# Kernel optimization log

Measured on AMD Instinct MI355X. Metric: run time of the kernel, lower is better.

Reference implementation:

```python
import jax, jax.numpy as jnp
import numpy as np

SL, BS, OUT_SL = 64, 64, 48
NH, EME, EMD = 256, 512, 768   # em_sz_dec == 3*NH required by copy-score reshape/bmm
VE, VD = 32000, 32000
NL = 2


def setup_inputs() -> dict:
    key = jax.random.key(0)
    ks = iter(jax.random.split(key, 32))
    def W(*s, sc=0.05):
        return jax.random.normal(next(ks), s, jnp.float32) * sc
    inp = jax.random.randint(next(ks), (SL, BS), 0, VE)
    y = jax.random.randint(next(ks), (SL, BS), 0, VD)
    return dict(
        inp=inp, y=y,
        emb_enc=W(VE, EME, sc=0.1),
        enc_Wih=W(NL, 2, 3 * NH, EME), enc_Whh=W(NL, 2, 3 * NH, NH),
        enc_bih=W(NL, 2, 3 * NH), enc_bhh=W(NL, 2, 3 * NH),
        out_enc_W=W(EMD, 2 * NH),
        emb_dec=W(VD, EMD, sc=0.1),
        dec_Wih=W(NL, 3 * EMD, EMD), dec_Whh=W(NL, 3 * EMD, EMD),
        dec_bih=W(NL, 3 * EMD), dec_bhh=W(NL, 3 * EMD),
        out_b=W(VD),
        W1=W(2 * NH, EMD), l2_W=W(EMD, EMD), l2_b=W(EMD),
        l3_W=W(EMD, EMD + 2 * NH), l3_b=W(EMD),
        Vp=W(EMD),
    )


def _gru_cell(x, h, Wih, Whh, bih, bhh):
    # torch nn.GRU cell equations
    gi = x @ Wih.T + bih
    gh = h @ Whh.T + bhh
    ir, iz, inn = jnp.split(gi, 3, axis=-1)
    hr, hz, hn = jnp.split(gh, 3, axis=-1)
    r = jax.nn.sigmoid(ir + hr)
    z = jax.nn.sigmoid(iz + hz)
    n = jnp.tanh(inn + r * hn)
    return (1.0 - z) * n + z * h


def _gru_layer(xs, h0, Wih, Whh, bih, bhh, reverse=False):
    def step(h, x):
        h2 = _gru_cell(x, h, Wih, Whh, bih, bhh)
        return h2, h2
    hT, ys = jax.lax.scan(step, h0, xs, reverse=reverse)
    return ys, hT


def reference(inp, y, emb_enc, enc_Wih, enc_Whh, enc_bih, enc_bhh, out_enc_W,
              emb_dec, dec_Wih, dec_Whh, dec_bih, dec_bhh, out_b,
              W1, l2_W, l2_b, l3_W, l3_b, Vp):
    sl, bs = inp.shape
    # ---- encoder: 2-layer bidirectional GRU ----
    x = emb_enc[inp]                                   # (sl, bs, EME)
    h_fin = []
    for l in range(NL):
        yf, hf = _gru_layer(x, jnp.zeros((bs, NH), x.dtype),
                            enc_Wih[l, 0], enc_Whh[l, 0], enc_bih[l, 0], enc_bhh[l, 0])
        yb, hb = _gru_layer(x, jnp.zeros((bs, NH), x.dtype),
                            enc_Wih[l, 1], enc_Whh[l, 1], enc_bih[l, 1], enc_bhh[l, 1],
                            reverse=True)
        x = jnp.concatenate([yf, yb], -1)              # (sl, bs, 2*NH)
        h_fin.append(jnp.concatenate([hf, hb], -1))    # (bs, 2*NH)
    enc_out = x
    # h.view(2,2,bs,-1).permute(0,2,1,3).view(2,bs,-1) == per-layer [fwd,bwd] concat
    h = jnp.stack(h_fin) @ out_enc_W.T                 # (2, bs, EMD)

    w1e = enc_out @ W1                                 # (sl, bs, EMD)
    sc_base = jnp.tanh(enc_out @ out_enc_W.T).transpose(1, 0, 2)  # (bs, sl, EMD)
    yT = y.T                                           # (bs, sl) copy indices
    Vsz = emb_dec.shape[0]
    row = jnp.arange(bs)[:, None]
    # dec_inp: step 0 uses zeros token, then teacher-forced y[i-1]
    dec_inputs = jnp.concatenate([jnp.zeros((1, bs), y.dtype), y[:OUT_SL - 1]], 0)

    def step(h, dec_t):
        # Bahdanau attention
        w2h = h[-1] @ l2_W.T + l2_b                    # (bs, EMD)
        u = jnp.tanh(w1e + w2h[None])                  # (sl, bs, EMD)
        a = jax.nn.softmax(u @ Vp, axis=0)             # (sl, bs)
        Xa = jnp.einsum('sb,sbe->be', a, enc_out)      # (bs, 2*NH)
        e = emb_dec[dec_t]                             # (bs, EMD)
        wgt = jnp.concatenate([e, Xa], -1) @ l3_W.T + l3_b
        # 2-layer decoder GRU, single step
        h0n = _gru_cell(wgt, h[0], dec_Wih[0], dec_Whh[0], dec_bih[0], dec_bhh[0])
        h1n = _gru_cell(h0n, h[1], dec_Wih[1], dec_Whh[1], dec_bih[1], dec_bhh[1])
        hn = jnp.stack([h0n, h1n])
        dec_out = h1n                                  # (bs, EMD)
        outp = dec_out @ emb_dec.T + out_b             # generate scores (bs, VD), tied weights
        score_c = jnp.tanh(jnp.einsum('bse,be->bs', sc_base, dec_out))  # copy scores (bs, sl)
        probs = jax.nn.softmax(jnp.concatenate([outp, score_c], 1), axis=1)  # (bs, VD+sl)
        prob_g = probs[:, :Vsz]
        prob_c = probs[:, Vsz:]
        # scatter-add copy probs onto the token ids of y (the copy mechanism)
        out1 = jnp.zeros_like(probs).at[row, yT].add(prob_c)
        out1 = out1.at[:, :Vsz].add(prob_g)
        return hn, out1

    _, res = jax.lax.scan(step, h, dec_inputs)         # (OUT_SL, bs, VD+sl)
    return res
```

## Files before the change

kernel.cpp:

```cpp
#include <hip/hip_runtime.h>

#define SLEN 64
#define BSZ  64
#define TSL  48
#define VDIM 32000
#define NCOL 32064

typedef __attribute__((ext_vector_type(8))) _Float16 f16x8;
typedef __attribute__((ext_vector_type(4))) _Float16 f16x4;
typedef __attribute__((ext_vector_type(4))) float f32x4;

__device__ __forceinline__ float fsig(float x){
    return 1.0f/(1.0f + __expf(-x));
}
__device__ __forceinline__ float ftanh(float x){
    float e = __expf(2.0f*x);
    return 1.0f - 2.0f/(e + 1.0f);
}
__device__ __forceinline__ unsigned short f2h(float x){
    union { _Float16 f; unsigned short u; } c; c.f = (_Float16)x; return c.u;
}
__device__ __forceinline__ float h2f(unsigned short u){
    union { _Float16 f; unsigned short u; } c; c.u = u; return (float)c.f;
}
// ... 226 lines not shown
    for (int g = 0; g < 3; ++g) acc[g] = (f32x4){0.f,0.f,0.f,0.f};

    const float* Ar = A + (size_t)arow*K + kof;
    const int brow_n = colg16 + (ln & 15);
    const int Khalf = K >> 1;
    const int kbeg = kh * Khalf;

    #pragma unroll 2
    for (int k0 = kbeg; k0 < kbeg + Khalf; k0 += 32) {
        float4 a0 = *reinterpret_cast<const float4*>(Ar + k0);
        float4 a1 = *reinterpret_cast<const float4*>(Ar + k0 + 4);
        f16x8 ah, al;
        {
            float av0=a0.x, av1=a0.y, av2=a0.z, av3=a0.w;
            float av4=a1.x, av5=a1.y, av6=a1.z, av7=a1.w;
            _Float16 hh;
            hh=(_Float16)av0; ah[0]=hh; al[0]=(_Float16)(av0-(float)hh);
            hh=(_Float16)av1; ah[1]=hh; al[1]=(_Float16)(av1-(float)hh);
            hh=(_Float16)av2; ah[2]=hh; al[2]=(_Float16)(av2-(float)hh);
            hh=(_Float16)av3; ah[3]=hh; al[3]=(_Float16)(av3-(float)hh);
            hh=(_Float16)av4; ah[4]=hh; al[4]=(_Float16)(av4-(float)hh);
            hh=(_Float16)av5; ah[5]=hh; al[5]=(_Float16)(av5-(float)hh);
            hh=(_Float16)av6; ah[6]=hh; al[6]=(_Float16)(av6-(float)hh);
            hh=(_Float16)av7; ah[7]=hh; al[7]=(_Float16)(av7-(float)hh);
        }
        #pragma unroll
        for (int g = 0; g < 3; ++g) {
            const size_t boff = (size_t)(g*768 + brow_n)*K + k0 + kof;
            f16x8 bh = *reinterpret_cast<const f16x8*>(&BH[boff]);
            acc[g] = __builtin_amdgcn_mfma_f32_16x16x32_f16(ah, bh, acc[g], 0,0,0);
            acc[g] = __builtin_amdgcn_mfma_f32_16x16x32_f16(al, bh, acc[g], 0,0,0);
            if (has_lo) {
                f16x8 bl = *reinterpret_cast<const f16x8*>(&BL[boff]);
                acc[g] = __builtin_amdgcn_mfma_f32_16x16x32_f16(ah, bl, acc[g], 0,0,0);
            }
        }
    }

    __shared__ float red[4][64][12];
    if (kh == 1) {
        #pragma unroll
        for (int g = 0; g < 3; ++g)
            #pragma unroll
            for (int j = 0; j < 4; ++j) red[rw][ln][g*4 + j] = acc[g][j];
    }
    __syncthreads();
    if (kh == 1) return;
    #pragma unroll
    for (int g = 0; g < 3; ++g)
        #pragma unroll
        for (int j = 0; j < 4; ++j) acc[g][j] += red[rw][ln][g*4 + j];

    const int colg = colg16 + (ln & 15);
    const int rb   = rw*16 + (ln >> 4)*4;
    if (gate) {
        const float br = bias[colg], bz = bias[768+colg], bn = bias[1536+colg];
        #pragma unroll
        for (int jj = 0; jj < 4; ++jj) {
            const int row = rb + jj;
            float er = 0.f, ez = 0.f, en = 0.f;
            if (E) {
                er = h2f(E[(size_t)row*2304 + colg]);
                ez = h2f(E[(size_t)row*2304 + 768 + colg]);
                en = h2f(E[(size_t)row*2304 + 1536 + colg]);
            }
            float ghr = gh[(size_t)row*2304 + colg];
            float ghz = gh[(size_t)row*2304 + 768 + colg];
            float ghn = gh[(size_t)row*2304 + 1536 + colg];
            float h   = hold[(size_t)row*768 + colg];
            outp[(size_t)row*768 + colg] =
                gru_fuse(acc[0][jj]+br+er, acc[1][jj]+bz+ez, acc[2][jj]+bn+en, ghr, ghz, ghn, h);
        }
    } else {
        #pragma unroll
        for (int g = 0; g < 3; ++g) {
            const float bz = bias[g*768 + colg];
            #pragma unroll
            for (int jj = 0; jj < 4; ++jj)
                outp[(size_t)(rb+jj)*2304 + g*768 + colg] = acc[g][jj] + bz;
        }
    }
}

__global__ __launch_bounds__(512) void vocab4_k(
    const float* __restrict__ A,
    const unsigned short* __restrict__ B0, const float* __restrict__ bias0,
    unsigned short* __restrict__ scr16, float* __restrict__ psum,
    const unsigned short* __restrict__ B1, const float* __restrict__ bias1, float* __restrict__ C1,
    const unsigned short* __restrict__ B2, const float* __restrict__ bias2, float* __restrict__ C2,
    const unsigned short* __restrict__ scb16, float* __restrict__ cpt)
{
    const int z = blockIdx.z;
    const int t = threadIdx.x, w = t >> 6, ln = t & 63;

    if (z == 3) {
        const int b = blockIdx.x;
        if (b >= 64) return;
        __shared__ float hsh[768];
        for (int i = t; i < 768; i += 512) hsh[i] = A[(size_t)b*768 + i];
        __syncthreads();
        for (int ss = 0; ss < 8; ++ss) {
            const int s = w*8 + ss;
            const unsigned short* sp = scb16 + (size_t)(b*64 + s)*768;
            float acc = 0.f;
            #pragma unroll
            for (int q = 0; q < 6; ++q) {
                int e = ln*2 + q*128;
                unsigned u = *reinterpret_cast<const unsigned*>(&sp[e]);
                acc += h2f((unsigned short)(u & 0xffff))*hsh[e]
                     + h2f((unsigned short)(u >> 16))*hsh[e+1];
            }
            for (int off = 32; off; off >>= 1) acc += __shfl_down(acc, off);
            if (ln == 0) cpt[b*64 + s] = ftanh(acc);
        }
        return;
    }

    const unsigned short* Bh; const float* bias; int N, ldc;
    if (z == 0)      { Bh=B0; bias=bias0; N=VDIM; ldc=VDIM; }
    else if (z == 1) { Bh=B1; bias=bias1; N=768;  ldc=768; }
    else             { Bh=B2; bias=bias2; N=2304; ldc=2304; }
    const int n0 = blockIdx.x * 128;
    if (n0 >= N) return;

    __shared__ __align__(16) unsigned short As[2][64][72];
    __shared__ __align__(16) unsigned short Bs[128][72];
    __shared__ float rs[4][64];

    const int cw = w & 3;
    const int mh = w >> 2;

    f32x4 acc[2][2];
    #pragma unroll
    for (int i = 0; i < 2; ++i)
        #pragma unroll
        for (int j = 0; j < 2; ++j) acc[i][j] = (f32x4){0.f,0.f,0.f,0.f};

    for (int k0 = 0; k0 < 768; k0 += 64) {
        __syncthreads();
        #pragma unroll
        for (int it = 0; it < 2; ++it) {
            int idx = t + it*512;
            int r = idx >> 4, c4 = (idx & 15) * 4;
            float4 v = *reinterpret_cast<const float4*>(A + (size_t)r*768 + k0 + c4);
            ushort4 h, l; float rm;
            h.x = f2h_hi(v.x, rm); l.x = f2h(rm);
            h.y = f2h_hi(v.y, rm); l.y = f2h(rm);
            h.z = f2h_hi(v.z, rm); l.z = f2h(rm);
            h.w = f2h_hi(v.w, rm); l.w = f2h(rm);
            *reinterpret_cast<ushort4*>(&As[0][r][c4]) = h;
            *reinterpret_cast<ushort4*>(&As[1][r][c4]) = l;
        }
        #pragma unroll
        for (int it = 0; it < 2; ++it) {
            int idx = t + it*512;
            int r = idx >> 3, c8 = (idx & 7) * 8;
            *reinterpret_cast<uint4*>(&Bs[r][c8]) =
                *reinterpret_cast<const uint4*>(&Bh[(size_t)(n0+r)*768 + k0 + c8]);
        }
        __syncthreads();
        #pragma unroll
        for (int ks = 0; ks < 2; ++ks) {
            const int ko = ks*32 + (ln >> 4)*8;
            f16x8 ah[2], al[2], bh[2];
            #pragma unroll
            for (int m = 0; m < 2; ++m) {
                ah[m] = *reinterpret_cast<const f16x8*>(&As[0][mh*32 + m*16 + (ln&15)][ko]);
                al[m] = *reinterpret_cast<const f16x8*>(&As[1][mh*32 + m*16 + (ln&15)][ko]);
            }
            #pragma unroll
            for (int n = 0; n < 2; ++n)
                bh[n] = *reinterpret_cast<const f16x8*>(&Bs[cw*32 + n*16 + (ln&15)][ko]);
            #pragma unroll
            for (int m = 0; m < 2; ++m)
                #pragma unroll
                for (int n = 0; n < 2; ++n) {
                    acc[m][n] = __builtin_amdgcn_mfma_f32_16x16x32_f16(ah[m], bh[n], acc[m][n], 0,0,0);
                    acc[m][n] = __builtin_amdgcn_mfma_f32_16x16x32_f16(al[m], bh[n], acc[m][n], 0,0,0);
                }
        }
    }

    if (z == 0) {
        __syncthreads();
        unsigned short (*Cs)[128] = reinterpret_cast<unsigned short(*)[128]>(&As[0][0][0]);
        float sums[2][4];
        #pragma unroll
        for (int m = 0; m < 2; ++m)
            #pragma unroll
            for (int j = 0; j < 4; ++j) sums[m][j] = 0.f;
        #pragma unroll
        for (int m = 0; m < 2; ++m) {
            #pragma unroll
            for (int n = 0; n < 2; ++n) {
                const int cl = cw*32 + n*16 + (ln & 15);
                const float bz = bias[n0 + cl];
                #pragma unroll
                for (int j = 0; j < 4; ++j) {
                    const int row = mh*32 + m*16 + (ln >> 4)*4 + j;
                    float e = __expf(acc[m][n][j] + bz);
                    Cs[row][cl] = f2h(e);
                    sums[m][j] += e;
                }
            }
        }
        #pragma unroll
        for (int m = 0; m < 2; ++m)
            #pragma unroll
            for (int j = 0; j < 4; ++j) {
                float v = sums[m][j];
                v += __shfl_xor(v, 1); v += __shfl_xor(v, 2);
                v += __shfl_xor(v, 4); v += __shfl_xor(v, 8);
                if ((ln & 15) == 0)
                    rs[cw][mh*32 + m*16 + (ln >> 4)*4 + j] = v;
            }
        __syncthreads();
        #pragma unroll
        for (int it = 0; it < 2; ++it) {
            int jj = t + it*512;
            int row = jj >> 4, c8 = (jj & 15) * 8;
            *reinterpret_cast<uint4*>(&scr16[(size_t)row*VDIM + n0 + c8]) =
                *reinterpret_cast<const uint4*>(&Cs[row][c8]);
        }
        if (t < 64)
            atomicAdd(&psum[t*8 + (blockIdx.x & 7)], rs[0][t]+rs[1][t]+rs[2][t]+rs[3][t]);
    } else {
        float* C = (z == 1) ? C1 : C2;
        #pragma unroll
        for (int m = 0; m < 2; ++m) {
            #pragma unroll
            for (int n = 0; n < 2; ++n) {
                const int col = n0 + cw*32 + n*16 + (ln & 15);
                const float bz = bias[col];
                #pragma unroll
                for (int j = 0; j < 4; ++j) {
                    const int row = mh*32 + m*16 + (ln >> 4)*4 + j;
                    C[(size_t)row*ldc + col] = acc[m][n][j] + bz;
                }
            }
        }
    }
}

__global__ __launch_bounds__(512) void attsm_k(
    const unsigned short* __restrict__ w1e16, const float* __restrict__ w2h,
    const float* __restrict__ Vp, const unsigned short* __restrict__ enc16,
    const int* __restrict__ y,
    int step, int do_att, int do_sm,
    float* __restrict__ wgt_in,
    const unsigned short* __restrict__ scr16, const float* __restrict__ cpt,
    const float* __restrict__ psum, float* __restrict__ outprev)
{
    const int b = blockIdx.x, t = threadIdx.x;
    const int w = t >> 6, ln = t & 63;
    if (blockIdx.y == 0) {
        if (!do_att) return;
        __shared__ float w2s[768];
        __shared__ float vps[768];
        __shared__ float aa[64];
        for (int i = t; i < 768; i += 512) { w2s[i] = w2h[(size_t)b*768 + i]; vps[i] = Vp[i]; }
        __syncthreads();
        for (int ss = 0; ss < 8; ++ss) {
            const int s = w*8 + ss;
            const unsigned short* wrow = w1e16 + (size_t)(b*64 + s)*768;
            float acc = 0.f;
            #pragma unroll
            for (int q = 0; q < 6; ++q) {
                int e = ln*2 + q*128;
                unsigned u = *reinterpret_cast<const unsigned*>(&wrow[e]);
                acc += ftanh(h2f((unsigned short)(u & 0xffff)) + w2s[e])*vps[e]
                     + ftanh(h2f((unsigned short)(u >> 16))   + w2s[e+1])*vps[e+1];
            }
            for (int off = 32; off; off >>= 1) acc += __shfl_down(acc, off);
            if (ln == 0) aa[s] = acc;
        }
        __syncthreads();
        if (t < 64) {
            float v = aa[t];
            float m = v;
            for (int off = 32; off; off >>= 1) m = fmaxf(m, __shfl_xor(m, off));
            float e = __expf(v - m);
            float ssum = e;
            for (int off = 32; off; off >>= 1) ssum += __shfl_xor(ssum, off);
            aa[t] = e / ssum;
        }
        __syncthreads();
        {
            float a0 = 0.f;
            const unsigned short* ebase = enc16 + (size_t)(b*64)*512 + t;
            #pragma unroll 8
            for (int s = 0; s < 64; ++s)
                a0 += aa[s] * h2f(ebase[(size_t)s*512]);
            wgt_in[(size_t)b*512 + t] = a0;
        }
    } else {
        if (!do_sm) return;
        __shared__ float cps[64];
        __shared__ float invS;
        if (t < 64) cps[t] = __expf(cpt[b*64 + t]);
        __syncthreads();
        if (t < 64) {
            float v = cps[t];
            for (int off = 32; off; off >>= 1) v += __shfl_xor(v, off);
            if (t == 0) {
                float tot = v;
                #pragma unroll
                for (int k = 0; k < 8; ++k) tot += psum[b*8 + k];
                invS = 1.0f / tot;
            }
        }
        __syncthreads();
        const float inv = invS;
        const unsigned short* srow = scr16 + (size_t)b*VDIM;
        float* orow = outprev + (size_t)b*NCOL;
        for (int i = t*8; i < VDIM; i += 4096) {
            uint4 u = *reinterpret_cast<const uint4*>(&srow[i]);
            float4 o0, o1;
            o0.x = h2f((unsigned short)(u.x & 0xffff))*inv; o0.y = h2f((unsigned short)(u.x >> 16))*inv;
            o0.z = h2f((unsigned short)(u.y & 0xffff))*inv; o0.w = h2f((unsigned short)(u.y >> 16))*inv;
            o1.x = h2f((unsigned short)(u.z & 0xffff))*inv; o1.y = h2f((unsigned short)(u.z >> 16))*inv;
            o1.z = h2f((unsigned short)(u.w & 0xffff))*inv; o1.w = h2f((unsigned short)(u.w >> 16))*inv;
            *reinterpret_cast<float4*>(&orow[i])     = o0;
            *reinterpret_cast<float4*>(&orow[i + 4]) = o1;
        }
        if (t >= 448) orow[VDIM + (t - 448)] = 0.0f;
        __syncthreads();
        if (t < 64) atomicAdd(&orow[y[t*64 + b]], cps[t] * inv);
    }
}

__global__ __launch_bounds__(256) void convhl_k(
    const float* __restrict__ W, unsigned short* __restrict__ hi,
    unsigned short* __restrict__ lo, int n4)
{
    int i = blockIdx.x*256 + threadIdx.x;
    if (i >= n4) return;
    float4 v = reinterpret_cast<const float4*>(W)[i];
    ushort4 h, l; float r;
    h.x = f2h_hi(v.x, r); l.x = f2h(r);
    h.y = f2h_hi(v.y, r); l.y = f2h(r);
    h.z = f2h_hi(v.z, r); l.z = f2h(r);
    h.w = f2h_hi(v.w, r); l.w = f2h(r);
    reinterpret_cast<ushort4*>(hi)[i] = h;
    reinterpret_cast<ushort4*>(lo)[i] = l;
}
__global__ __launch_bounds__(256) void conv16_k(
    const float* __restrict__ W, unsigned short* __restrict__ hi, int n4)
{
    int i = blockIdx.x*256 + threadIdx.x;
    if (i >= n4) return;
    float4 v = reinterpret_cast<const float4*>(W)[i];
    ushort4 h;
    h.x = f2h(v.x); h.y = f2h(v.y); h.z = f2h(v.z); h.w = f2h(v.w);
    reinterpret_cast<ushort4*>(hi)[i] = h;
}
__global__ __launch_bounds__(256) void convw03_k(
    const float* __restrict__ W03f, unsigned short* __restrict__ We,
    unsigned short* __restrict__ Wx)
{
    int i = blockIdx.x*256 + threadIdx.x;
    if (i >= 2304*320) return;
    int r = i / 320, c4 = (i - r*320) * 4;
    float4 v = *reinterpret_cast<const float4*>(W03f + (size_t)r*1280 + c4);
    ushort4 h;
    h.x = f2h(v.x); h.y = f2h(v.y); h.z = f2h(v.z); h.w = f2h(v.w);
    if (c4 < 768)
        *reinterpret_cast<ushort4*>(&We[(size_t)r*768 + c4]) = h;
    else
        *reinterpret_cast<ushort4*>(&Wx[(size_t)r*512 + (c4 - 768)]) = h;
}
__global__ __launch_bounds__(256) void embrows_k(
    const int* __restrict__ y, const float* __restrict__ emb_dec,
    float* __restrict__ Ag)
{
    int i = blockIdx.x*256 + threadIdx.x;
    if (i >= 3072*192) return;
    int row = i / 192, c4 = (i - row*192) * 4;
    int tok = (row < 64) ? 0 : y[row - 64];
    *reinterpret_cast<float4*>(Ag + (size_t)row*768 + c4) =
        *reinterpret_cast<const float4*>(emb_dec + (size_t)tok*768 + c4);
}
__global__ __launch_bounds__(256) void transpose2_k(
    const float* __restrict__ S, float* __restrict__ D, int R, int C)
{
    int i = blockIdx.x*256 + threadIdx.x;
    if (i >= R*C) return;
    int r = i / C, c = i - r*C;
    D[(size_t)c*R + r] = S[i];
}
__global__ __launch_bounds__(256) void b03_k(
    const float* __restrict__ Wih0, const float* __restrict__ bih0,
    const float* __restrict__ l3b, float* __restrict__ b03)
{
    int j = blockIdx.x*256 + threadIdx.x;
    if (j >= 2304) return;
    const float* wr = Wih0 + (size_t)j*768;
    float s = 0.f;
    #pragma unroll 4
    for (int m = 0; m < 768; m += 4) {
        float4 w = *reinterpret_cast<const float4*>(wr + m);
        float4 b = *reinterpret_cast<const float4*>(l3b + m);
        s += w.x*b.x + w.y*b.y + w.z*b.z + w.w*b.w;
    }
    b03[j] = bih0[j] + s;
}

__global__ __launch_bounds__(256) void embed_k(const int* inp, const float* emb, float* x)
{
    int i = blockIdx.x*256 + threadIdx.x;
    if (i >= 4096*128) return;
// ... 247 lines not shown
        const int s = wv*16 + ss;
        const float* sp = scb + (size_t)(b*64 + s)*768;
        float acc = 0.f;
        #pragma unroll
        for (int q = 0; q < 12; ++q) { int e = ln + q*64; acc += sp[e]*hsh[e]; }
        for (int off = 32; off; off >>= 1) acc += __shfl_down(acc, off);
        if (ln == 0) cps[s] = ftanh(acc);
    }
    __syncthreads();

    const float* row = scratch + (size_t)b*VDIM;
    float m = -1e30f;
    for (int i = t; i < VDIM; i += 256) m = fmaxf(m, row[i]);
    for (int off = 32; off; off >>= 1) m = fmaxf(m, __shfl_xor(m, off));
    if (ln == 0) red[wv] = m;
    __syncthreads();
    const float bm = fmaxf(fmaxf(red[0], red[1]), fmaxf(red[2], red[3]));
    __syncthreads();

    float s = 0.f;
    for (int i = t; i < VDIM; i += 256) s += __expf(row[i] - bm);
    if (t < 64) s += __expf(cps[t] - bm);
    for (int off = 32; off; off >>= 1) s += __shfl_xor(s, off);
    if (ln == 0) red[wv] = s;
    __syncthreads();
    const float inv = 1.0f / (red[0] + red[1] + red[2] + red[3]);

    float* orow = out + (size_t)b*NCOL;
    for (int i = t; i < VDIM; i += 256) orow[i] = __expf(row[i] - bm) * inv;
    if (t >= 192) orow[VDIM + (t - 192)] = 0.0f;
    __syncthreads();
    if (t < 64) atomicAdd(&orow[y[t*64 + b]], __expf(cps[t] - bm) * inv);
}

extern "C" void kernel_launch(void* const* d_in, const int* in_sizes, int n_in,
                              void* d_out, int out_size, void* d_ws, size_t ws_size,
                              hipStream_t stream)
{
    (void)in_sizes; (void)n_in; (void)out_size;
    const int*   inp       = (const int*)  d_in[0];
    const int*   y         = (const int*)  d_in[1];
    const float* emb_enc   = (const float*)d_in[2];
    const float* enc_Wih   = (const float*)d_in[3];
    const float* enc_Whh   = (const float*)d_in[4];
    const float* enc_bih   = (const float*)d_in[5];
    const float* enc_bhh   = (const float*)d_in[6];
    const float* out_enc_W = (const float*)d_in[7];
    const float* emb_dec   = (const float*)d_in[8];
    const float* dec_Wih   = (const float*)d_in[9];
    const float* dec_Whh   = (const float*)d_in[10];
    const float* dec_bih   = (const float*)d_in[11];
    const float* dec_bhh   = (const float*)d_in[12];
    const float* out_b     = (const float*)d_in[13];
    const float* W1        = (const float*)d_in[14];
    const float* l2_W      = (const float*)d_in[15];
    const float* l2_b      = (const float*)d_in[16];
    const float* l3_W      = (const float*)d_in[17];
    const float* l3_b      = (const float*)d_in[18];
    const float* Vp        = (const float*)d_in[19];
    float* out = (float*)d_out;
    float* ws  = (float*)d_ws;

    size_t off = 0;
    auto alloc = [&](size_t n) { float* p = ws + off; off += (n + 63) & ~(size_t)63; return p; };
    float* x0     = alloc(4096*512);
    float* x1     = alloc(4096*512);
    float* x2     = alloc(4096*512);
    float* giF    = alloc(4096*768);
    float* giB    = alloc(4096*768);
    float* w1e    = alloc(4096*768);
    float* scb    = alloc(4096*768);
    float* W1T    = alloc(768*512);
    float* hfin   = alloc(128*512);
    float* hdecA  = alloc(128*768);
    float* hdecB  = alloc(128*768);
    float* w2h    = alloc(64*768);
    float* wgt_in = alloc(64*1280);
    float* wgt    = alloc(64*768);
    float* gh0buf = alloc(64*2304);
    float* gh1buf = alloc(64*2304);
    float* gi0f   = alloc(64*2304);
    float* gi1f   = alloc(64*2304);
    float* b03    = alloc(2304);
    float* psum   = alloc(512);
    float* cpt    = alloc(64*64);
    float* scratch= alloc(64*VDIM);
    auto ualloc = [&](size_t nush) { return (unsigned short*)alloc((nush + 1) / 2); };
    unsigned short* encWhhH = ualloc(2*2*768*256);
    unsigned short* encWhhP = ualloc(2*3*32*256*8);
    unsigned short* embH    = ualloc((size_t)VDIM*768);
    unsigned short* encWihH = ualloc(2*2*768*512);
    unsigned short* encWihL = ualloc(2*2*768*512);
    unsigned short* W1TH    = ualloc(768*512);
    unsigned short* W1TL    = ualloc(768*512);
    unsigned short* oeH     = ualloc(768*512);
    unsigned short* oeL     = ualloc(768*512);
    unsigned short* l2H     = ualloc(768*768);
    unsigned short* l3TH    = ualloc(1280*768);
    unsigned short* l3TL    = ualloc(1280*768);
    unsigned short* dWihH   = ualloc((size_t)2*2304*768);
    unsigned short* dWhhH   = ualloc((size_t)2*2304*768);
    unsigned short* W03eH   = ualloc((size_t)2304*768);
    unsigned short* W03xH   = ualloc((size_t)2304*512);
    unsigned short* Egi16   = ualloc((size_t)3072*2304);
    const bool use_mfma = ws_size >= off * sizeof(float);

    const size_t L1W = (size_t)2304*768;
    float* l3T  = scratch;
    float* W03f = x0;
    float* Ag   = x0;
    unsigned short* scr16 = (unsigned short*)scratch;
    unsigned short* w1e16 = (unsigned short*)giF;
    unsigned short* enc16 = (unsigned short*)(giF + 1600*1024);
    unsigned short* scb16 = (unsigned short*)giB;

    embed_k<<<2048, 256, 0, stream>>>(inp, emb_enc, x0);
    transpose2_k<<<(512*768 + 255)/256, 256, 0, stream>>>(W1, W1T, 512, 768);
    conv16_k<<<768, 256, 0, stream>>>(enc_Whh, encWhhH, 2*2*768*256/4);

    if (use_mfma) {
        packwhh_k<<<192, 256, 0, stream>>>(enc_Whh, encWhhP);
        convhl_k<<<1536, 256, 0, stream>>>(enc_Wih, encWihH, encWihL, 2*2*768*512/4);
        convhl_k<<<384, 256, 0, stream>>>(W1T, W1TH, W1TL, 768*512/4);
        convhl_k<<<384, 256, 0, stream>>>(out_enc_W, oeH, oeL, 768*512/4);
        conv16_k<<<576, 256, 0, stream>>>(l2_W, l2H, 768*768/4);
        conv16_k<<<3456, 256, 0, stream>>>(dec_Wih, dWihH, (int)(L1W*2/4));
        conv16_k<<<3456, 256, 0, stream>>>(dec_Whh, dWhhH, (int)(L1W*2/4));
        conv16_k<<<24000, 256, 0, stream>>>(emb_dec, embH, (int)((size_t)VDIM*768/4));
        transpose2_k<<<(768*1280 + 255)/256, 256, 0, stream>>>(l3_W, l3T, 768, 1280);
        convhl_k<<<960, 256, 0, stream>>>(l3T, l3TH, l3TL, 1280*768/4);
        b03_k<<<9, 256, 0, stream>>>(dec_Wih, dec_bih, l3_b, b03);

        for (int l = 0; l < 2; ++l) {
            const float* xin  = l ? x1 : x0;
            float*       xout = l ? x2 : x1;
            const size_t wo = (size_t)l*2*768*512;
            mfma_gemm<<<dim3(6, 64, 2), 256, 0, stream>>>(
                xin, encWihH + wo,           encWihL + wo,           enc_bih + l*2*768,       giF, 768, 768, 0,
                xin, encWihH + wo + 768*512, encWihL + wo + 768*512, enc_bih + l*2*768 + 768, giB, 768, 768, 0,
                512, 0);
            enc_cp_k<<<dim3(64, 2), 256, 0, stream>>>(
                giF, giB, encWhhP, enc_bhh + (size_t)l*2*768,
                xout, hfin + (size_t)l*64*512, l);
            if (l == 0)
                packwhh_k<<<192, 256, 0, stream>>>(enc_Whh + (size_t)2*768*256, encWhhP);
        }

        mfma_gemm<<<dim3(10, 36, 1), 256, 0, stream>>>(
            dec_Wih, l3TH, l3TL, nullptr, W03f, 1280, 1280, 0,
            nullptr, nullptr, nullptr, nullptr, nullptr, 0, 0, 0,
            768, 0);
        convw03_k<<<(2304*320 + 255)/256, 256, 0, stream>>>(W03f, W03eH, W03xH);

        embrows_k<<<(3072*192 + 255)/256, 256, 0, stream>>>(y, emb_dec, Ag);
        mfma_gemm<<<dim3(18, 48, 1), 256, 0, stream>>>(
            Ag, W03eH, nullptr, nullptr, (float*)Egi16, 2304, 2304, 0,
            nullptr, nullptr, nullptr, nullptr, nullptr, 0, 0, 0,
            768, 1);

        mfma_gemm<<<dim3(6, 2, 1), 256, 0, stream>>>(
            hfin, oeH, oeL, nullptr, hdecA, 768, 768, 0,
            nullptr, nullptr, nullptr, nullptr, nullptr, 0, 0, 0,
            512, 0);

        mfma_gemm<<<dim3(6, 64, 2), 256, 0, stream>>>(
            x2, W1TH, W1TL, nullptr, w1e, 768, 768, 0,
            x2, oeH,  oeL,  nullptr, scb, 768, 768, 1,
            512, 0);

        conv16_k<<<3072, 256, 0, stream>>>(w1e, w1e16, 4096*768/4);
        conv16_k<<<3072, 256, 0, stream>>>(scb, scb16, 4096*768/4);
        conv16_k<<<2048, 256, 0, stream>>>(x2, enc16, 4096*512/4);

        mfma_gemm<<<dim3(6, 1, 1), 256, 0, stream>>>(
            hdecA + 64*768, l2H, nullptr, l2_b, w2h, 768, 768, 0,
            nullptr, nullptr, nullptr, nullptr, nullptr, 0, 0, 0,
            768, 0);
        gru_mfma_k<<<dim3(48, 1, 2), 512, 0, stream>>>(
            hdecA,          dWhhH,       nullptr, dec_bhh,        nullptr, nullptr, gh0buf, 0, 768, nullptr,
            hdecA + 64*768, dWhhH + L1W, nullptr, dec_bhh + 2304, nullptr, nullptr, gh1buf, 0, 768, nullptr,
            nullptr);

        for (int st = 0; st < TSL; ++st) {
            float* h0c = (st & 1) ? hdecB : hdecA;
            float* h0n = (st & 1) ? hdecA : hdecB;
            float* h1c = h0c + 64*768;
            float* h1n = h0n + 64*768;
            float* oprev = out + (size_t)(st > 0 ? st - 1 : 0)*BSZ*NCOL;

            attsm_k<<<dim3(64, 2), 512, 0, stream>>>(
                w1e16, w2h, Vp, enc16, y, st, 1, (st > 0) ? 1 : 0,
                wgt_in, scr16, cpt, psum, oprev);

            gru_mfma_k<<<dim3(48, 1, 1), 512, 0, stream>>>(
                wgt_in, W03xH, nullptr, b03, gh0buf, h0c, h0n, 1, 512, Egi16 + (size_t)st*64*2304,
                wgt_in, W03xH, nullptr, b03, gh0buf, h0c, h0n, 1, 512, Egi16 + (size_t)st*64*2304,
                psum);

            gru_mfma_k<<<dim3(48, 1, 2), 512, 0, stream>>>(
                h0n, dWihH + L1W, nullptr, dec_bih + 2304, gh1buf, h1c, h1n, 1, 768, nullptr,
                h0n, dWhhH,       nullptr, dec_bhh,        nullptr, nullptr, gh0buf, 0, 768, nullptr,
                nullptr);

            vocab4_k<<<dim3(250, 1, 4), 512, 0, stream>>>(
                h1n,
                embH, out_b, scr16, psum,
                l2H, l2_b, w2h,
                dWhhH + L1W, dec_bhh + 2304, gh1buf,
                scb16, cpt);
        }
        attsm_k<<<dim3(64, 2), 512, 0, stream>>>(
            w1e16, w2h, Vp, enc16, y, TSL, 0, 1,
            wgt_in, scr16, cpt, psum, out + (size_t)(TSL-1)*BSZ*NCOL);
    } else {
        for (int l = 0; l < 2; ++l) {
            const float* xin  = l ? x1 : x0;
            float*       xout = l ? x2 : x1;
            const float* Wih = enc_Wih + (size_t)l*2*768*512;
            const float* bih = enc_bih + (size_t)l*2*768;
            gemm64<<<dim3(12, 64, 2), 256, 0, stream>>>(
                xin, Wih,           bih,       giF, 0,
                xin, Wih + 768*512, bih + 768, giB, 0,
                4096, 768, 512, 768);
            enc_layer4_k<<<dim3(16, 2), 256, 0, stream>>>(
                giF, giB, encWhhH + (size_t)l*2*768*256, enc_bhh + (size_t)l*2*768,
                xout, hfin + (size_t)l*64*512, l);
        }
        gemm64<<<dim3(12, 2, 1), 256, 0, stream>>>(
            hfin, out_enc_W, nullptr, hdecA, 0,
            hfin, out_enc_W, nullptr, hdecA, 0,
            128, 768, 512, 768);
        gemm64<<<dim3(12, 64, 2), 256, 0, stream>>>(
            x2, W1T,       nullptr, w1e, 0,
            x2, out_enc_W, nullptr, scb, 1,
            4096, 768, 512, 768);
        gemm_skinny<<<dim3(12, 4, 1), 256, 0, stream>>>(
            hdecA + 64*768, l2_W, l2_b, w2h,
            hdecA + 64*768, l2_W, l2_b, w2h,
            768, 768, 768);

        for (int st = 0; st < TSL; ++st) {
            float* h0c = (st & 1) ? hdecB : hdecA;
            float* h0n = (st & 1) ? hdecA : hdecB;
            float* h1c = h0c + 64*768;
            float* h1n = h0n + 64*768;
            float* orow = out + (size_t)st*BSZ*NCOL;

            att_fused_k<<<64, 256, 0, stream>>>(w1e, w2h, Vp, x2, emb_dec, y, st, wgt_in);
            gemm_skinny<<<dim3(12, 4, 1), 256, 0, stream>>>(
                wgt_in, l3_W, l3_b, wgt,
                wgt_in, l3_W, l3_b, wgt,
                768, 1280, 768);
            gemm_skinny<<<dim3(36, 4, 2), 256, 0, stream>>>(
                wgt, dec_Wih, dec_bih, gi0f,
                h0c, dec_Whh, dec_bhh, gh0buf,
                2304, 768, 2304);
            gru_gate_k<<<192, 256, 0, stream>>>(gi0f, gh0buf, h0c, h0n);
            gemm_skinny<<<dim3(36, 4, 2), 256, 0, stream>>>(
                h0n, dec_Wih + L1W, dec_bih + 2304, gi1f,
                h1c, dec_Whh + L1W, dec_bhh + 2304, gh1buf,
                2304, 768, 2304);
            gru_gate_k<<<192, 256, 0, stream>>>(gi1f, gh1buf, h1c, h1n);
            gemm_skinny<<<dim3(12, 4, 1), 256, 0, stream>>>(
                h1n, l2_W, l2_b, w2h,
                h1n, l2_W, l2_b, w2h,
                768, 768, 768);
            gemm64<<<dim3(500, 1, 1), 256, 0, stream>>>(
                h1n, emb_dec, out_b, scratch, 0,
                h1n, emb_dec, out_b, scratch, 0,
                64, VDIM, 768, VDIM);
            smax2_k<<<64, 256, 0, stream>>>(scratch, scb, h1n, y, orow);
        }
    }
}
```

Before: 5.063 ms.

## Software-pipeline vocab GEMM one step behind and fuse it with attention

Moves the large vocab-projection GEMM out of the per-step tail kernel and into a merged kernel that runs next step's attention and the previous step's softmax normalisation/scatter in the same launch. The vocab GEMM for step st-1 now overlaps with attention for step st, and normalisation lags two steps, so scratch, psum and copy-score buffers are double-buffered. The aim is to shorten the serial critical path of the decoder loop by letting the independent vocab work fill the GPU during the small latency-bound attention and GRU kernels. It costs a second 64x32000 fp16 scratch buffer and two extra drain launches after the loop.

```diff
diff --git a/kernel.cpp b/kernel.cpp
--- a/kernel.cpp
+++ b/kernel.cpp
@@ -332,20 +332,217 @@
     }
 }
 
-__global__ __launch_bounds__(512) void vocab4_k(
+__global__ __launch_bounds__(512) void mega_k(
+    const float* __restrict__ hv, const unsigned short* __restrict__ embH,
+    const float* __restrict__ out_b,
+    unsigned short* __restrict__ scrW, float* __restrict__ psumW,
+    const unsigned short* __restrict__ w1e16, const float* __restrict__ w2h,
+    const float* __restrict__ Vp, const unsigned short* __restrict__ enc16,
+    float* __restrict__ wgt_in,
+    const unsigned short* __restrict__ scrR, const float* __restrict__ cptR,
+    const float* __restrict__ psumR,
+    const int* __restrict__ y, float* __restrict__ outprev,
+    int do_vocab, int do_att, int do_sm)
+{
+    __shared__ __align__(16) unsigned short As[2][64][72];
+    __shared__ __align__(16) unsigned short Bs[128][72];
+    __shared__ float rs[4][64];
+    const int bid = blockIdx.x;
+    const int t = threadIdx.x, w = t >> 6, ln = t & 63;
+
+    if (bid < 250) {
+        if (!do_vocab) return;
+        const int n0 = bid * 128;
+        const int cw = w & 3, mh = w >> 2;
+
+        f32x4 acc[2][2];
+        #pragma unroll
+        for (int i = 0; i < 2; ++i)
+            #pragma unroll
+            for (int j = 0; j < 2; ++j) acc[i][j] = (f32x4){0.f,0.f,0.f,0.f};
+
+        for (int k0 = 0; k0 < 768; k0 += 64) {
+            __syncthreads();
+            #pragma unroll
+            for (int it = 0; it < 2; ++it) {
+                int idx = t + it*512;
+                int r = idx >> 4, c4 = (idx & 15) * 4;
+                float4 v = *reinterpret_cast<const float4*>(hv + (size_t)r*768 + k0 + c4);
+                ushort4 h, l; float rm;
+                h.x = f2h_hi(v.x, rm); l.x = f2h(rm);
+                h.y = f2h_hi(v.y, rm); l.y = f2h(rm);
+                h.z = f2h_hi(v.z, rm); l.z = f2h(rm);
+                h.w = f2h_hi(v.w, rm); l.w = f2h(rm);
+                *reinterpret_cast<ushort4*>(&As[0][r][c4]) = h;
+                *reinterpret_cast<ushort4*>(&As[1][r][c4]) = l;
+            }
+            #pragma unroll
+            for (int it = 0; it < 2; ++it) {
+                int idx = t + it*512;
+                int r = idx >> 3, c8 = (idx & 7) * 8;
+                *reinterpret_cast<uint4*>(&Bs[r][c8]) =
+                    *reinterpret_cast<const uint4*>(&embH[(size_t)(n0+r)*768 + k0 + c8]);
+            }
+            __syncthreads();
+            #pragma unroll
+            for (int ks = 0; ks < 2; ++ks) {
+                const int ko = ks*32 + (ln >> 4)*8;
+                f16x8 ah[2], al[2], bh[2];
+                #pragma unroll
+                for (int m = 0; m < 2; ++m) {
+                    ah[m] = *reinterpret_cast<const f16x8*>(&As[0][mh*32 + m*16 + (ln&15)][ko]);
+                    al[m] = *reinterpret_cast<const f16x8*>(&As[1][mh*32 + m*16 + (ln&15)][ko]);
+                }
+                #pragma unroll
+                for (int n = 0; n < 2; ++n)
+                    bh[n] = *reinterpret_cast<const f16x8*>(&Bs[cw*32 + n*16 + (ln&15)][ko]);
+                #pragma unroll
+                for (int m = 0; m < 2; ++m)
+                    #pragma unroll
+                    for (int n = 0; n < 2; ++n) {
+                        acc[m][n] = __builtin_amdgcn_mfma_f32_16x16x32_f16(ah[m], bh[n], acc[m][n], 0,0,0);
+                        acc[m][n] = __builtin_amdgcn_mfma_f32_16x16x32_f16(al[m], bh[n], acc[m][n], 0,0,0);
+                    }
+            }
+        }
+
+        __syncthreads();
+        unsigned short (*Cs)[128] = reinterpret_cast<unsigned short(*)[128]>(&As[0][0][0]);
+        float sums[2][4];
+        #pragma unroll
+        for (int m = 0; m < 2; ++m)
+            #pragma unroll
+            for (int j = 0; j < 4; ++j) sums[m][j] = 0.f;
+        #pragma unroll
+        for (int m = 0; m < 2; ++m) {
+            #pragma unroll
+            for (int n = 0; n < 2; ++n) {
+                const int cl = cw*32 + n*16 + (ln & 15);
+                const float bz = out_b[n0 + cl];
+                #pragma unroll
+                for (int j = 0; j < 4; ++j) {
+                    const int row = mh*32 + m*16 + (ln >> 4)*4 + j;
+                    float e = __expf(acc[m][n][j] + bz);
+                    Cs[row][cl] = f2h(e);
+                    sums[m][j] += e;
+                }
+            }
+        }
+        #pragma unroll
+        for (int m = 0; m < 2; ++m)
+            #pragma unroll
+            for (int j = 0; j < 4; ++j) {
+                float v = sums[m][j];
+                v += __shfl_xor(v, 1); v += __shfl_xor(v, 2);
+                v += __shfl_xor(v, 4); v += __shfl_xor(v, 8);
+                if ((ln & 15) == 0)
+                    rs[cw][mh*32 + m*16 + (ln >> 4)*4 + j] = v;
+            }
+        __syncthreads();
+        #pragma unroll
+        for (int it = 0; it < 2; ++it) {
+            int jj = t + it*512;
+            int row = jj >> 4, c8 = (jj & 15) * 8;
+            *reinterpret_cast<uint4*>(&scrW[(size_t)row*VDIM + n0 + c8]) =
+                *reinterpret_cast<const uint4*>(&Cs[row][c8]);
+        }
+        if (t < 64)
+            atomicAdd(&psumW[t*8 + (bid & 7)], rs[0][t]+rs[1][t]+rs[2][t]+rs[3][t]);
+        return;
+    }
+
+    if (bid < 314) {
+        if (!do_att) return;
+        const int b = bid - 250;
+        float* w2s = (float*)&As[0][0][0];
+        float* vps = w2s + 768;
+        float* aa  = vps + 768;
+        for (int i = t; i < 768; i += 512) { w2s[i] = w2h[(size_t)b*768 + i]; vps[i] = Vp[i]; }
+        __syncthreads();
+        for (int ss = 0; ss < 8; ++ss) {
+            const int s = w*8 + ss;
+            const unsigned short* wrow = w1e16 + (size_t)(b*64 + s)*768;
+            float acc = 0.f;
+            #pragma unroll
+            for (int q = 0; q < 6; ++q) {
+                int e = ln*2 + q*128;
+                unsigned u = *reinterpret_cast<const unsigned*>(&wrow[e]);
+                acc += ftanh(h2f((unsigned short)(u & 0xffff)) + w2s[e])*vps[e]
+                     + ftanh(h2f((unsigned short)(u >> 16))   + w2s[e+1])*vps[e+1];
+            }
+            for (int off = 32; off; off >>= 1) acc += __shfl_down(acc, off);
+            if (ln == 0) aa[s] = acc;
+        }
+        __syncthreads();
+        if (t < 64) {
+            float v = aa[t];
+            float m = v;
+            for (int off = 32; off; off >>= 1) m = fmaxf(m, __shfl_xor(m, off));
+            float e = __expf(v - m);
+            float ssum = e;
+            for (int off = 32; off; off >>= 1) ssum += __shfl_xor(ssum, off);
+            aa[t] = e / ssum;
+        }
+        __syncthreads();
+        {
+            float a0 = 0.f;
+            const unsigned short* ebase = enc16 + (size_t)(b*64)*512 + t;
+            #pragma unroll 8
+            for (int s = 0; s < 64; ++s)
+                a0 += aa[s] * h2f(ebase[(size_t)s*512]);
+            wgt_in[(size_t)b*512 + t] = a0;
+        }
+        return;
+    }
+
+    {
+        if (!do_sm) return;
+        const int b = bid - 314;
+        float* cps = (float*)&As[0][0][0];
+        float* pinv = cps + 64;
+        if (t < 64) cps[t] = __expf(cptR[b*64 + t]);
+        __syncthreads();
+        if (t < 64) {
+            float v = cps[t];
+            for (int off = 32; off; off >>= 1) v += __shfl_xor(v, off);
+            if (t == 0) {
+                float tot = v;
+                #pragma unroll
+                for (int k = 0; k < 8; ++k) tot += psumR[b*8 + k];
+                *pinv = 1.0f / tot;
+            }
+        }
+        __syncthreads();
+        const float inv = *pinv;
+        const unsigned short* srow = scrR + (size_t)b*VDIM;
+        float* orow = outprev + (size_t)b*NCOL;
+        for (int i = t*8; i < VDIM; i += 4096) {
+            uint4 u = *reinterpret_cast<const uint4*>(&srow[i]);
+            float4 o0, o1;
+            o0.x = h2f((unsigned short)(u.x & 0xffff))*inv; o0.y = h2f((unsigned short)(u.x >> 16))*inv;
+            o0.z = h2f((unsigned short)(u.y & 0xffff))*inv; o0.w = h2f((unsigned short)(u.y >> 16))*inv;
+            o1.x = h2f((unsigned short)(u.z & 0xffff))*inv; o1.y = h2f((unsigned short)(u.z >> 16))*inv;
+            o1.z = h2f((unsigned short)(u.w & 0xffff))*inv; o1.w = h2f((unsigned short)(u.w >> 16))*inv;
+            *reinterpret_cast<float4*>(&orow[i])     = o0;
+            *reinterpret_cast<float4*>(&orow[i + 4]) = o1;
+        }
+        if (t >= 448) orow[VDIM + (t - 448)] = 0.0f;
+        __syncthreads();
+        if (t < 64) atomicAdd(&orow[y[t*64 + b]], cps[t] * inv);
+    }
+}
+
+__global__ __launch_bounds__(512) void vocabD_k(
     const float* __restrict__ A,
-    const unsigned short* __restrict__ B0, const float* __restrict__ bias0,
-    unsigned short* __restrict__ scr16, float* __restrict__ psum,
     const unsigned short* __restrict__ B1, const float* __restrict__ bias1, float* __restrict__ C1,
     const unsigned short* __restrict__ B2, const float* __restrict__ bias2, float* __restrict__ C2,
     const unsigned short* __restrict__ scb16, float* __restrict__ cpt)
 {
-    const int z = blockIdx.z;
+    const int bid = blockIdx.x;
     const int t = threadIdx.x, w = t >> 6, ln = t & 63;
 
-    if (z == 3) {
-        const int b = blockIdx.x;
-        if (b >= 64) return;
+    if (bid >= 24) {
+        const int b = bid - 24;
         __shared__ float hsh[768];
         for (int i = t; i < 768; i += 512) hsh[i] = A[(size_t)b*768 + i];
         __syncthreads();
@@ -366,19 +563,13 @@
         return;
     }
 
-    const unsigned short* Bh; const float* bias; int N, ldc;
-    if (z == 0)      { Bh=B0; bias=bias0; N=VDIM; ldc=VDIM; }
-    else if (z == 1) { Bh=B1; bias=bias1; N=768;  ldc=768; }
-    else             { Bh=B2; bias=bias2; N=2304; ldc=2304; }
-    const int n0 = blockIdx.x * 128;
-    if (n0 >= N) return;
+    const unsigned short* Bh; const float* bias; float* C; int n0, ldc;
+    if (bid < 6) { Bh=B1; bias=bias1; C=C1; n0=bid*128; ldc=768; }
+    else         { Bh=B2; bias=bias2; C=C2; n0=(bid-6)*128; ldc=2304; }
 
     __shared__ __align__(16) unsigned short As[2][64][72];
     __shared__ __align__(16) unsigned short Bs[128][72];
-    __shared__ float rs[4][64];
-
-    const int cw = w & 3;
-    const int mh = w >> 2;
+    const int cw = w & 3, mh = w >> 2;
 
     f32x4 acc[2][2];
     #pragma unroll
@@ -431,151 +622,18 @@
         }
     }
 
-    if (z == 0) {
-        __syncthreads();
-        unsigned short (*Cs)[128] = reinterpret_cast<unsigned short(*)[128]>(&As[0][0][0]);
-        float sums[2][4];
-        #pragma unroll
-        for (int m = 0; m < 2; ++m)
-            #pragma unroll
-            for (int j = 0; j < 4; ++j) sums[m][j] = 0.f;
-        #pragma unroll
-        for (int m = 0; m < 2; ++m) {
-            #pragma unroll
-            for (int n = 0; n < 2; ++n) {
-                const int cl = cw*32 + n*16 + (ln & 15);
-                const float bz = bias[n0 + cl];
-                #pragma unroll
-                for (int j = 0; j < 4; ++j) {
-                    const int row = mh*32 + m*16 + (ln >> 4)*4 + j;
-                    float e = __expf(acc[m][n][j] + bz);
-                    Cs[row][cl] = f2h(e);
-                    sums[m][j] += e;
-                }
-            }
-        }
-        #pragma unroll
-        for (int m = 0; m < 2; ++m)
+    #pragma unroll
+    for (int m = 0; m < 2; ++m) {
+        #pragma unroll
+        for (int n = 0; n < 2; ++n) {
+            const int col = n0 + cw*32 + n*16 + (ln & 15);
+            const float bz = bias[col];
             #pragma unroll
             for (int j = 0; j < 4; ++j) {
-                float v = sums[m][j];
-                v += __shfl_xor(v, 1); v += __shfl_xor(v, 2);
-                v += __shfl_xor(v, 4); v += __shfl_xor(v, 8);
-                if ((ln & 15) == 0)
-                    rs[cw][mh*32 + m*16 + (ln >> 4)*4 + j] = v;
-            }
-        __syncthreads();
-        #pragma unroll
-        for (int it = 0; it < 2; ++it) {
-            int jj = t + it*512;
-            int row = jj >> 4, c8 = (jj & 15) * 8;
-            *reinterpret_cast<uint4*>(&scr16[(size_t)row*VDIM + n0 + c8]) =
-                *reinterpret_cast<const uint4*>(&Cs[row][c8]);
-        }
-        if (t < 64)
-            atomicAdd(&psum[t*8 + (blockIdx.x & 7)], rs[0][t]+rs[1][t]+rs[2][t]+rs[3][t]);
-    } else {
-        float* C = (z == 1) ? C1 : C2;
-        #pragma unroll
-        for (int m = 0; m < 2; ++m) {
-            #pragma unroll
-            for (int n = 0; n < 2; ++n) {
-                const int col = n0 + cw*32 + n*16 + (ln & 15);
-                const float bz = bias[col];
-                #pragma unroll
-                for (int j = 0; j < 4; ++j) {
-                    const int row = mh*32 + m*16 + (ln >> 4)*4 + j;
-                    C[(size_t)row*ldc + col] = acc[m][n][j] + bz;
-                }
-            }
-        }
-    }
-}
-
-__global__ __launch_bounds__(512) void attsm_k(
-    const unsigned short* __restrict__ w1e16, const float* __restrict__ w2h,
-    const float* __restrict__ Vp, const unsigned short* __restrict__ enc16,
-    const int* __restrict__ y,
-    int step, int do_att, int do_sm,
-    float* __restrict__ wgt_in,
-    const unsigned short* __restrict__ scr16, const float* __restrict__ cpt,
-    const float* __restrict__ psum, float* __restrict__ outprev)
-{
-    const int b = blockIdx.x, t = threadIdx.x;
-    const int w = t >> 6, ln = t & 63;
-    if (blockIdx.y == 0) {
-        if (!do_att) return;
-        __shared__ float w2s[768];
-        __shared__ float vps[768];
-        __shared__ float aa[64];
-        for (int i = t; i < 768; i += 512) { w2s[i] = w2h[(size_t)b*768 + i]; vps[i] = Vp[i]; }
-        __syncthreads();
-        for (int ss = 0; ss < 8; ++ss) {
-            const int s = w*8 + ss;
-            const unsigned short* wrow = w1e16 + (size_t)(b*64 + s)*768;
-            float acc = 0.f;
-            #pragma unroll
-            for (int q = 0; q < 6; ++q) {
-                int e = ln*2 + q*128;
-                unsigned u = *reinterpret_cast<const unsigned*>(&wrow[e]);
-                acc += ftanh(h2f((unsigned short)(u & 0xffff)) + w2s[e])*vps[e]
-                     + ftanh(h2f((unsigned short)(u >> 16))   + w2s[e+1])*vps[e+1];
-            }
-            for (int off = 32; off; off >>= 1) acc += __shfl_down(acc, off);
-            if (ln == 0) aa[s] = acc;
-        }
-        __syncthreads();
-        if (t < 64) {
-            float v = aa[t];
-            float m = v;
-            for (int off = 32; off; off >>= 1) m = fmaxf(m, __shfl_xor(m, off));
-            float e = __expf(v - m);
-            float ssum = e;
-            for (int off = 32; off; off >>= 1) ssum += __shfl_xor(ssum, off);
-            aa[t] = e / ssum;
-        }
-        __syncthreads();
-        {
-            float a0 = 0.f;
-            const unsigned short* ebase = enc16 + (size_t)(b*64)*512 + t;
-            #pragma unroll 8
-            for (int s = 0; s < 64; ++s)
-                a0 += aa[s] * h2f(ebase[(size_t)s*512]);
-            wgt_in[(size_t)b*512 + t] = a0;
-        }
-    } else {
-        if (!do_sm) return;
-        __shared__ float cps[64];
-        __shared__ float invS;
-        if (t < 64) cps[t] = __expf(cpt[b*64 + t]);
-        __syncthreads();
-        if (t < 64) {
-            float v = cps[t];
-            for (int off = 32; off; off >>= 1) v += __shfl_xor(v, off);
-            if (t == 0) {
-                float tot = v;
-                #pragma unroll
-                for (int k = 0; k < 8; ++k) tot += psum[b*8 + k];
-                invS = 1.0f / tot;
-            }
-        }
-        __syncthreads();
-        const float inv = invS;
-        const unsigned short* srow = scr16 + (size_t)b*VDIM;
-        float* orow = outprev + (size_t)b*NCOL;
-        for (int i = t*8; i < VDIM; i += 4096) {
-            uint4 u = *reinterpret_cast<const uint4*>(&srow[i]);
-            float4 o0, o1;
-            o0.x = h2f((unsigned short)(u.x & 0xffff))*inv; o0.y = h2f((unsigned short)(u.x >> 16))*inv;
-            o0.z = h2f((unsigned short)(u.y & 0xffff))*inv; o0.w = h2f((unsigned short)(u.y >> 16))*inv;
-            o1.x = h2f((unsigned short)(u.z & 0xffff))*inv; o1.y = h2f((unsigned short)(u.z >> 16))*inv;
-            o1.z = h2f((unsigned short)(u.w & 0xffff))*inv; o1.w = h2f((unsigned short)(u.w >> 16))*inv;
-            *reinterpret_cast<float4*>(&orow[i])     = o0;
-            *reinterpret_cast<float4*>(&orow[i + 4]) = o1;
-        }
-        if (t >= 448) orow[VDIM + (t - 448)] = 0.0f;
-        __syncthreads();
-        if (t < 64) atomicAdd(&orow[y[t*64 + b]], cps[t] * inv);
+                const int row = mh*32 + m*16 + (ln >> 4)*4 + j;
+                C[(size_t)row*ldc + col] = acc[m][n][j] + bz;
+            }
+        }
     }
 }
 
@@ -989,8 +1047,8 @@
     float* gi0f   = alloc(64*2304);
     float* gi1f   = alloc(64*2304);
     float* b03    = alloc(2304);
-    float* psum   = alloc(512);
-    float* cpt    = alloc(64*64);
+    float* psum   = alloc(1024);
+    float* cpt    = alloc(2*4096);
     float* scratch= alloc(64*VDIM);
     auto ualloc = [&](size_t nush) { return (unsigned short*)alloc((nush + 1) / 2); };
     unsigned short* encWhhH = ualloc(2*2*768*256);
@@ -1013,6 +1071,7 @@
     const bool use_mfma = ws_size >= off * sizeof(float);
 
     const size_t L1W = (size_t)2304*768;
+    const size_t SCR = (size_t)64*VDIM;
     float* l3T  = scratch;
     float* W03f = x0;
     float* Ag   = x0;
@@ -1093,32 +1152,50 @@
             float* h0n = (st & 1) ? hdecA : hdecB;
             float* h1c = h0c + 64*768;
             float* h1n = h0n + 64*768;
-            float* oprev = out + (size_t)(st > 0 ? st - 1 : 0)*BSZ*NCOL;
-
-            attsm_k<<<dim3(64, 2), 512, 0, stream>>>(
-                w1e16, w2h, Vp, enc16, y, st, 1, (st > 0) ? 1 : 0,
-                wgt_in, scr16, cpt, psum, oprev);
+
+            mega_k<<<378, 512, 0, stream>>>(
+                h1c, embH, out_b,
+                scr16 + ((st+1)&1)*SCR, psum + ((st+1)&1)*512,
+                w1e16, w2h, Vp, enc16, wgt_in,
+                scr16 + (st&1)*SCR, cpt + (st&1)*4096, psum + (st&1)*512,
+                y, out + (size_t)(st >= 2 ? st-2 : 0)*BSZ*NCOL,
+                st >= 1, 1, st >= 2);
 
             gru_mfma_k<<<dim3(48, 1, 1), 512, 0, stream>>>(
                 wgt_in, W03xH, nullptr, b03, gh0buf, h0c, h0n, 1, 512, Egi16 + (size_t)st*64*2304,
                 wgt_in, W03xH, nullptr, b03, gh0buf, h0c, h0n, 1, 512, Egi16 + (size_t)st*64*2304,
-                psum);
+                psum + (st&1)*512);
 
             gru_mfma_k<<<dim3(48, 1, 2), 512, 0, stream>>>(
                 h0n, dWihH + L1W, nullptr, dec_bih + 2304, gh1buf, h1c, h1n, 1, 768, nullptr,
                 h0n, dWhhH,       nullptr, dec_bhh,        nullptr, nullptr, gh0buf, 0, 768, nullptr,
                 nullptr);
 
-            vocab4_k<<<dim3(250, 1, 4), 512, 0, stream>>>(
+            vocabD_k<<<88, 512, 0, stream>>>(
                 h1n,
-                embH, out_b, scr16, psum,
                 l2H, l2_b, w2h,
                 dWhhH + L1W, dec_bhh + 2304, gh1buf,
-                scb16, cpt);
-        }
-        attsm_k<<<dim3(64, 2), 512, 0, stream>>>(
-            w1e16, w2h, Vp, enc16, y, TSL, 0, 1,
-            wgt_in, scr16, cpt, psum, out + (size_t)(TSL-1)*BSZ*NCOL);
+                scb16, cpt + (st&1)*4096);
+        }
+        {
+            int st = TSL;
+            float* h1c = ((st & 1) ? hdecB : hdecA) + 64*768;
+            mega_k<<<378, 512, 0, stream>>>(
+                h1c, embH, out_b,
+                scr16 + ((st+1)&1)*SCR, psum + ((st+1)&1)*512,
+                w1e16, w2h, Vp, enc16, wgt_in,
+                scr16 + (st&1)*SCR, cpt + (st&1)*4096, psum + (st&1)*512,
+                y, out + (size_t)(st-2)*BSZ*NCOL,
+                1, 0, 1);
+            st = TSL + 1;
+            mega_k<<<378, 512, 0, stream>>>(
+                nullptr, embH, out_b,
+                scr16 + ((st+1)&1)*SCR, psum + ((st+1)&1)*512,
+                w1e16, w2h, Vp, enc16, wgt_in,
+                scr16 + (st&1)*SCR, cpt + (st&1)*4096, psum + (st&1)*512,
+                y, out + (size_t)(st-2)*BSZ*NCOL,
+                0, 0, 1);
+        }
     } else {
         for (int l = 0; l < 2; ++l) {
             const float* xin  = l ? x1 : x0;
```

After: 5.127 ms. Within noise of the previous version (+1.3%).
